# Optimization experiments

Hardware: AMD Instinct MI355X
Metric: run time of the kernel (lower is better)

Reference implementation:

```python
import jax, jax.numpy as jnp
import numpy as np

LEFT = 16  # attention window size (previous `left` symbols incl. current)


def _make_history(symbols, left):
    """contexts[b, t, j] = symbols[b, t - (left-1-j)] for j in [0,left),
    padded with symbols[b, 0] for out-of-range positions (pad = symbols[:, :1])."""
    B, T = symbols.shape
    # (T, left) gather index matrix
    idx = jnp.arange(T)[:, None] - (left - 1 - jnp.arange(left))[None, :]
    valid = idx >= 0
    idx_c = jnp.clip(idx, 0, T - 1)
    ctx = symbols[:, idx_c]                                   # (B, T, left)
    pad = symbols[:, :1][:, :, None]                          # (B, 1, 1)
    return jnp.where(valid[None, :, :], ctx, pad)             # (B, T, left)


def setup_inputs() -> dict:
    key = jax.random.key(0)
    k1, k2, k3, k4 = jax.random.split(key, 4)
    B, T, V, D = 8, 2048, 256, 512
    symbols = jax.random.randint(k1, (B, T), 0, V, dtype=jnp.int32)
    encodings = jax.random.normal(k2, (B, T, D), dtype=jnp.float32)
    # keras 'uniform' initializer: U(-0.05, 0.05)
    M = jax.random.uniform(k3, (V, D), minval=-0.05, maxval=0.05, dtype=jnp.float32)
    C = jax.random.uniform(k4, (V, D), minval=-0.05, maxval=0.05, dtype=jnp.float32)
    return {"symbols": symbols, "encodings": encodings, "M": M, "C": C}


def reference(symbols, encodings, M, C):
    contexts = _make_history(symbols, LEFT)                   # (B, T, L) int
    Mg = M[contexts]                                          # (B, T, L, D)
    Cg = C[contexts]                                          # (B, T, L, D)
    scores = jnp.einsum('btld,btd->btl', Mg, encodings)       # (B, T, L)
    p = jax.nn.softmax(scores, axis=-1)                       # (B, T, L)
    compressed = jnp.einsum('btl,btld->btd', p, Cg)           # (B, T, D)
    output = jnp.concatenate([compressed, encodings], axis=-1)  # (B, T, 2D)
    return output, p
```

## Files before the change

### kernel.cpp

```cpp
#include <hip/hip_runtime.h>
#include <hip/hip_bf16.h>

#define B_ 8
#define T_ 2048
#define V_ 256
#define D_ 512
#define LEFT_ 16

typedef float f32x4 __attribute__((ext_vector_type(4)));
typedef short bf16x8 __attribute__((ext_vector_type(8)));
union FragU { unsigned u[4]; bf16x8 v; };

__device__ __forceinline__ unsigned pack_bf2(float a, float b) {
    __hip_bfloat162 h = __float22bfloat162_rn(make_float2(a, b));
    union { __hip_bfloat162 h; unsigned u; } c; c.h = h; return c.u;
}

__global__ __launch_bounds__(512)
void score_kernel(const int* __restrict__ symbols,
                  const float* __restrict__ encodings,
                  const float* __restrict__ M,
                  float* __restrict__ out,
                  float* __restrict__ p_out) {
    __shared__ __align__(16) float sp[8 * 16 * 36];

    const int tid  = threadIdx.x;
    const int lane = tid & 63;
    const int w    = tid >> 6;
    const int q    = lane >> 4;
    const int t    = lane & 15;

    const int blk = blockIdx.x;
    const int b   = blk >> 7;
    const int t0  = (blk & 127) * 16;
    const int* symrow = symbols + b * T_;
    const size_t rowbase = (size_t)b * T_ + t0;

    int sa[2];
    #pragma unroll
    for (int g = 0; g < 2; ++g) {
        int pos = t0 + t + 16 * g - (LEFT_ - 1);
        pos = max(pos, 0); pos = min(pos, T_ - 1);
        sa[g] = symrow[pos];
    }

    FragU bf[2];
    {
        const float* ebase = encodings + (rowbase + t) * D_;
        float* obase = out + (rowbase + t) * 1024 + D_;
        #pragma unroll
        for (int kc = 0; kc < 2; ++kc) {
            const int d0 = 64 * w + 32 * kc + 4 * q;
            const float4 e0 = *(const float4*)(ebase + d0);
            const float4 e1 = *(const float4*)(ebase + d0 + 16);
            *(float4*)(obase + d0)      = e0;
            *(float4*)(obase + d0 + 16) = e1;
            bf[kc].u[0] = pack_bf2(e0.x, e0.y); bf[kc].u[1] = pack_bf2(e0.z, e0.w);
            bf[kc].u[2] = pack_bf2(e1.x, e1.y); bf[kc].u[3] = pack_bf2(e1.z, e1.w);
        }
    }

    f32x4 acc0 = {0.f, 0.f, 0.f, 0.f}, acc1 = {0.f, 0.f, 0.f, 0.f};
    #pragma unroll
    for (int kc = 0; kc < 2; ++kc) {
        const int k0 = 64 * w + 32 * kc + 4 * q;
        {
            const float* ma = M + (size_t)sa[0] * D_ + k0;
            const float4 x0 = *(const float4*)ma;
            const float4 x1 = *(const float4*)(ma + 16);
            FragU af;
            af.u[0] = pack_bf2(x0.x, x0.y); af.u[1] = pack_bf2(x0.z, x0.w);
            af.u[2] = pack_bf2(x1.x, x1.y); af.u[3] = pack_bf2(x1.z, x1.w);
            acc0 = __builtin_amdgcn_mfma_f32_16x16x32_bf16(af.v, bf[kc].v, acc0, 0, 0, 0);
        }
        {
            const float* ma = M + (size_t)sa[1] * D_ + k0;
            const float4 x0 = *(const float4*)ma;
            const float4 x1 = *(const float4*)(ma + 16);
            FragU af;
            af.u[0] = pack_bf2(x0.x, x0.y); af.u[1] = pack_bf2(x0.z, x0.w);
            af.u[2] = pack_bf2(x1.x, x1.y); af.u[3] = pack_bf2(x1.z, x1.w);
            acc1 = __builtin_amdgcn_mfma_f32_16x16x32_bf16(af.v, bf[kc].v, acc1, 0, 0, 0);
        }
    }
    *(f32x4*)&sp[(w * 16 + t) * 36 + 4 * q]      = acc0;
    *(f32x4*)&sp[(w * 16 + t) * 36 + 16 + 4 * q] = acc1;

    __syncthreads();

    {
        f32x4 s0 = *(const f32x4*)&sp[t * 36 + 4 * q];
        f32x4 s1 = *(const f32x4*)&sp[t * 36 + 16 + 4 * q];
        #pragma unroll
        for (int w2 = 1; w2 < 8; ++w2) {
            s0 += *(const f32x4*)&sp[(w2 * 16 + t) * 36 + 4 * q];
            s1 += *(const f32x4*)&sp[(w2 * 16 + t) * 36 + 16 + 4 * q];
        }
        float mx = -3.0e38f;
        #pragma unroll
        for (int r = 0; r < 4; ++r) {
            if ((unsigned)(4 * q + r - t) < 16u)      mx = fmaxf(mx, s0[r]);
            if ((unsigned)(4 * q + r + 16 - t) < 16u) mx = fmaxf(mx, s1[r]);
        }
        mx = fmaxf(mx, __shfl_xor(mx, 16));
        mx = fmaxf(mx, __shfl_xor(mx, 32));
        float p0[4], p1[4];
        float sum = 0.f;
        #pragma unroll
        for (int r = 0; r < 4; ++r) {
            const bool m0 = (unsigned)(4 * q + r - t) < 16u;
            const bool m1 = (unsigned)(4 * q + r + 16 - t) < 16u;
            p0[r] = m0 ? __expf(s0[r] - mx) : 0.f;
            p1[r] = m1 ? __expf(s1[r] - mx) : 0.f;
            sum += p0[r] + p1[r];
        }
        sum += __shfl_xor(sum, 16);
        sum += __shfl_xor(sum, 32);
        const float inv = 1.f / sum;

        if (w == 0) {
            #pragma unroll
            for (int r = 0; r < 4; ++r) {
                const int j0 = 4 * q + r;
                if ((unsigned)(j0 - t) < 16u)
                    p_out[(rowbase + t) * 16 + (j0 - t)] = p0[r] * inv;
                else
                    p_out[(rowbase + t) * 16 + (j0 + 16 - t)] = p1[r] * inv;
            }
        }
    }
}

__global__ __launch_bounds__(256)
void compress_kernel(const int* __restrict__ symbols,
                     const float* __restrict__ C,
                     const float* __restrict__ p_in,
                     float* __restrict__ out) {
    const int tid  = threadIdx.x;
    const int lane = tid & 63;
    const int w    = tid >> 6;

    const int blk = blockIdx.x;
    const int b   = blk >> 7;
    const int tb  = (blk & 127) * 16 + w * 4;
    const int* symrow = symbols + b * T_;
    const size_t rowbase = (size_t)b * T_ + tb;
    const int dof = lane * 8;

    float pv[4];
    #pragma unroll
    for (int tk = 0; tk < 4; ++tk)
        pv[tk] = p_in[(rowbase + tk) * 16 + (lane & 15)];

    float4 a0[4], a1[4];
    #pragma unroll
    for (int tk = 0; tk < 4; ++tk) {
        a0[tk] = make_float4(0.f, 0.f, 0.f, 0.f);
        a1[tk] = make_float4(0.f, 0.f, 0.f, 0.f);
    }

    #pragma unroll
    for (int i = 0; i < 19; ++i) {
        int pos = tb - (LEFT_ - 1) + i;
        pos = max(pos, 0);
        const int sym = __builtin_amdgcn_readfirstlane(symrow[pos]);
        const float* cr = C + (size_t)sym * D_ + dof;
        const float4 c0 = *(const float4*)cr;
        const float4 c1 = *(const float4*)(cr + 4);
        #pragma unroll
        for (int tk = 0; tk < 4; ++tk) {
            const int sl = i - tk;
            if (sl >= 0 && sl < 16) {
                const float pb = __shfl(pv[tk], sl);
                a0[tk].x += pb * c0.x; a0[tk].y += pb * c0.y;
                a0[tk].z += pb * c0.z; a0[tk].w += pb * c0.w;
                a1[tk].x += pb * c1.x; a1[tk].y += pb * c1.y;
                a1[tk].z += pb * c1.z; a1[tk].w += pb * c1.w;
            }
        }
    }

    #pragma unroll
    for (int tk = 0; tk < 4; ++tk) {
        float* ob = out + (rowbase + tk) * 1024 + dof;
        *(float4*)ob       = a0[tk];
        *(float4*)(ob + 4) = a1[tk];
    }
}

extern "C" void kernel_launch(void* const* d_in, const int* in_sizes, int n_in,
                              void* d_out, int out_size, void* d_ws, size_t ws_size,
                              hipStream_t stream) {
    const int*   symbols   = (const int*)d_in[0];
    const float* encodings = (const float*)d_in[1];
    const float* M         = (const float*)d_in[2];
    const float* C         = (const float*)d_in[3];
    float* out   = (float*)d_out;
    float* p_out = out + (size_t)B_ * T_ * 1024;

    dim3 grid(B_ * (T_ / 16));
    score_kernel<<<grid, 512, 0, stream>>>(symbols, encodings, M, out, p_out);
    compress_kernel<<<grid, 256, 0, stream>>>(symbols, C, p_out, out);
}
```

Baseline: 39.90 us.

## Fuse score/softmax and compress kernels into one per-wave attention kernel

Merges the score and compress kernels into a single launch. Each wave now computes scores for its own 4 timesteps over the full D with 16 MFMA steps, which removes the cross-wave LDS reduction and __syncthreads. The probabilities stay in registers and are broadcast via shuffles into the compress loop, so p no longer round-trips through global memory and one launch is dropped. In exchange, each wave does redundant MFMA work because only 4 of the 16 columns are useful, and it loads more M rows per wave.

```diff
diff --git a/kernel.cpp b/kernel.cpp
--- a/kernel.cpp
+++ b/kernel.cpp
@@ -16,14 +16,13 @@
     union { __hip_bfloat162 h; unsigned u; } c; c.h = h; return c.u;
 }
 
-__global__ __launch_bounds__(512)
-void score_kernel(const int* __restrict__ symbols,
-                  const float* __restrict__ encodings,
-                  const float* __restrict__ M,
-                  float* __restrict__ out,
-                  float* __restrict__ p_out) {
-    __shared__ __align__(16) float sp[8 * 16 * 36];
-
+__global__ __launch_bounds__(256)
+void attn_cell_kernel(const int* __restrict__ symbols,
+                      const float* __restrict__ encodings,
+                      const float* __restrict__ M,
+                      const float* __restrict__ C,
+                      float* __restrict__ out,
+                      float* __restrict__ p_out) {
     const int tid  = threadIdx.x;
     const int lane = tid & 63;
     const int w    = tid >> 6;
@@ -32,125 +31,98 @@
 
     const int blk = blockIdx.x;
     const int b   = blk >> 7;
-    const int t0  = (blk & 127) * 16;
+    const int tb  = (blk & 127) * 16 + w * 4;
     const int* symrow = symbols + b * T_;
-    const size_t rowbase = (size_t)b * T_ + t0;
+    const size_t rowbase = (size_t)b * T_ + tb;
+    const int dof = lane * 8;
 
-    int sa[2];
+    int syms[19];
     #pragma unroll
-    for (int g = 0; g < 2; ++g) {
-        int pos = t0 + t + 16 * g - (LEFT_ - 1);
-        pos = max(pos, 0); pos = min(pos, T_ - 1);
-        sa[g] = symrow[pos];
+    for (int i = 0; i < 19; ++i) {
+        int pos = tb - (LEFT_ - 1) + i;
+        pos = max(pos, 0);
+        syms[i] = __builtin_amdgcn_readfirstlane(symrow[pos]);
     }
 
-    FragU bf[2];
+    #pragma unroll
+    for (int tk = 0; tk < 4; ++tk) {
+        const float* e = encodings + (rowbase + tk) * D_ + dof;
+        const float4 x0 = *(const float4*)e;
+        const float4 x1 = *(const float4*)(e + 4);
+        float* o = out + (rowbase + tk) * 1024 + D_ + dof;
+        *(float4*)o       = x0;
+        *(float4*)(o + 4) = x1;
+    }
+
+    int pos0 = tb - (LEFT_ - 1) + t;  pos0 = max(pos0, 0);
+    int pos1 = tb + 1 + min(t, 2);
+    const int sym0 = symrow[pos0];
+    const int sym1 = symrow[pos1];
+
+    f32x4 acc0 = {0.f, 0.f, 0.f, 0.f}, acc1 = {0.f, 0.f, 0.f, 0.f};
     {
-        const float* ebase = encodings + (rowbase + t) * D_;
-        float* obase = out + (rowbase + t) * 1024 + D_;
+        const float* eb  = encodings + (rowbase + (t & 3)) * D_;
+        const float* ma0 = M + (size_t)sym0 * D_;
+        const float* ma1 = M + (size_t)sym1 * D_;
         #pragma unroll
-        for (int kc = 0; kc < 2; ++kc) {
-            const int d0 = 64 * w + 32 * kc + 4 * q;
-            const float4 e0 = *(const float4*)(ebase + d0);
-            const float4 e1 = *(const float4*)(ebase + d0 + 16);
-            *(float4*)(obase + d0)      = e0;
-            *(float4*)(obase + d0 + 16) = e1;
-            bf[kc].u[0] = pack_bf2(e0.x, e0.y); bf[kc].u[1] = pack_bf2(e0.z, e0.w);
-            bf[kc].u[2] = pack_bf2(e1.x, e1.y); bf[kc].u[3] = pack_bf2(e1.z, e1.w);
+        for (int ks = 0; ks < 16; ++ks) {
+            const int k0 = ks * 32 + 4 * q;
+            const float4 e0 = *(const float4*)(eb + k0);
+            const float4 e1 = *(const float4*)(eb + k0 + 16);
+            FragU bf;
+            bf.u[0] = pack_bf2(e0.x, e0.y); bf.u[1] = pack_bf2(e0.z, e0.w);
+            bf.u[2] = pack_bf2(e1.x, e1.y); bf.u[3] = pack_bf2(e1.z, e1.w);
+            const float4 m00 = *(const float4*)(ma0 + k0);
+            const float4 m01 = *(const float4*)(ma0 + k0 + 16);
+            FragU a0;
+            a0.u[0] = pack_bf2(m00.x, m00.y); a0.u[1] = pack_bf2(m00.z, m00.w);
+            a0.u[2] = pack_bf2(m01.x, m01.y); a0.u[3] = pack_bf2(m01.z, m01.w);
+            const float4 m10 = *(const float4*)(ma1 + k0);
+            const float4 m11 = *(const float4*)(ma1 + k0 + 16);
+            FragU a1;
+            a1.u[0] = pack_bf2(m10.x, m10.y); a1.u[1] = pack_bf2(m10.z, m10.w);
+            a1.u[2] = pack_bf2(m11.x, m11.y); a1.u[3] = pack_bf2(m11.z, m11.w);
+            acc0 = __builtin_amdgcn_mfma_f32_16x16x32_bf16(a0.v, bf.v, acc0, 0, 0, 0);
+            acc1 = __builtin_amdgcn_mfma_f32_16x16x32_bf16(a1.v, bf.v, acc1, 0, 0, 0);
         }
     }
 
-    f32x4 acc0 = {0.f, 0.f, 0.f, 0.f}, acc1 = {0.f, 0.f, 0.f, 0.f};
-    #pragma unroll
-    for (int kc = 0; kc < 2; ++kc) {
-        const int k0 = 64 * w + 32 * kc + 4 * q;
-        {
-            const float* ma = M + (size_t)sa[0] * D_ + k0;
-            const float4 x0 = *(const float4*)ma;
-            const float4 x1 = *(const float4*)(ma + 16);
-            FragU af;
-            af.u[0] = pack_bf2(x0.x, x0.y); af.u[1] = pack_bf2(x0.z, x0.w);
-            af.u[2] = pack_bf2(x1.x, x1.y); af.u[3] = pack_bf2(x1.z, x1.w);
-            acc0 = __builtin_amdgcn_mfma_f32_16x16x32_bf16(af.v, bf[kc].v, acc0, 0, 0, 0);
-        }
-        {
-            const float* ma = M + (size_t)sa[1] * D_ + k0;
-            const float4 x0 = *(const float4*)ma;
-            const float4 x1 = *(const float4*)(ma + 16);
-            FragU af;
-            af.u[0] = pack_bf2(x0.x, x0.y); af.u[1] = pack_bf2(x0.z, x0.w);
-            af.u[2] = pack_bf2(x1.x, x1.y); af.u[3] = pack_bf2(x1.z, x1.w);
-            acc1 = __builtin_amdgcn_mfma_f32_16x16x32_bf16(af.v, bf[kc].v, acc1, 0, 0, 0);
-        }
-    }
-    *(f32x4*)&sp[(w * 16 + t) * 36 + 4 * q]      = acc0;
-    *(f32x4*)&sp[(w * 16 + t) * 36 + 16 + 4 * q] = acc1;
-
-    __syncthreads();
-
+    float p0[4], p1[4];
     {
-        f32x4 s0 = *(const f32x4*)&sp[t * 36 + 4 * q];
-        f32x4 s1 = *(const f32x4*)&sp[t * 36 + 16 + 4 * q];
-        #pragma unroll
-        for (int w2 = 1; w2 < 8; ++w2) {
-            s0 += *(const f32x4*)&sp[(w2 * 16 + t) * 36 + 4 * q];
-            s1 += *(const f32x4*)&sp[(w2 * 16 + t) * 36 + 16 + 4 * q];
-        }
         float mx = -3.0e38f;
         #pragma unroll
         for (int r = 0; r < 4; ++r) {
-            if ((unsigned)(4 * q + r - t) < 16u)      mx = fmaxf(mx, s0[r]);
-            if ((unsigned)(4 * q + r + 16 - t) < 16u) mx = fmaxf(mx, s1[r]);
+            if ((unsigned)(4 * q + r - t) < 16u)      mx = fmaxf(mx, acc0[r]);
+            if ((unsigned)(4 * q + r + 16 - t) < 16u) mx = fmaxf(mx, acc1[r]);
         }
         mx = fmaxf(mx, __shfl_xor(mx, 16));
         mx = fmaxf(mx, __shfl_xor(mx, 32));
-        float p0[4], p1[4];
         float sum = 0.f;
         #pragma unroll
         for (int r = 0; r < 4; ++r) {
             const bool m0 = (unsigned)(4 * q + r - t) < 16u;
             const bool m1 = (unsigned)(4 * q + r + 16 - t) < 16u;
-            p0[r] = m0 ? __expf(s0[r] - mx) : 0.f;
-            p1[r] = m1 ? __expf(s1[r] - mx) : 0.f;
+            p0[r] = m0 ? __expf(acc0[r] - mx) : 0.f;
+            p1[r] = m1 ? __expf(acc1[r] - mx) : 0.f;
             sum += p0[r] + p1[r];
         }
         sum += __shfl_xor(sum, 16);
         sum += __shfl_xor(sum, 32);
         const float inv = 1.f / sum;
+        #pragma unroll
+        for (int r = 0; r < 4; ++r) { p0[r] *= inv; p1[r] *= inv; }
+    }
 
-        if (w == 0) {
-            #pragma unroll
-            for (int r = 0; r < 4; ++r) {
-                const int j0 = 4 * q + r;
-                if ((unsigned)(j0 - t) < 16u)
-                    p_out[(rowbase + t) * 16 + (j0 - t)] = p0[r] * inv;
-                else
-                    p_out[(rowbase + t) * 16 + (j0 + 16 - t)] = p1[r] * inv;
-            }
+    if (t < 4) {
+        #pragma unroll
+        for (int r = 0; r < 4; ++r) {
+            const int j0 = 4 * q + r;
+            if ((unsigned)(j0 - t) < 16u)
+                p_out[(rowbase + t) * 16 + (j0 - t)] = p0[r];
+            else
+                p_out[(rowbase + t) * 16 + (j0 + 16 - t)] = p1[r];
         }
     }
-}
-
-__global__ __launch_bounds__(256)
-void compress_kernel(const int* __restrict__ symbols,
-                     const float* __restrict__ C,
-                     const float* __restrict__ p_in,
-                     float* __restrict__ out) {
-    const int tid  = threadIdx.x;
-    const int lane = tid & 63;
-    const int w    = tid >> 6;
-
-    const int blk = blockIdx.x;
-    const int b   = blk >> 7;
-    const int tb  = (blk & 127) * 16 + w * 4;
-    const int* symrow = symbols + b * T_;
-    const size_t rowbase = (size_t)b * T_ + tb;
-    const int dof = lane * 8;
-
-    float pv[4];
-    #pragma unroll
-    for (int tk = 0; tk < 4; ++tk)
-        pv[tk] = p_in[(rowbase + tk) * 16 + (lane & 15)];
 
     float4 a0[4], a1[4];
     #pragma unroll
@@ -158,20 +130,18 @@
         a0[tk] = make_float4(0.f, 0.f, 0.f, 0.f);
         a1[tk] = make_float4(0.f, 0.f, 0.f, 0.f);
     }
-
     #pragma unroll
     for (int i = 0; i < 19; ++i) {
-        int pos = tb - (LEFT_ - 1) + i;
-        pos = max(pos, 0);
-        const int sym = __builtin_amdgcn_readfirstlane(symrow[pos]);
-        const float* cr = C + (size_t)sym * D_ + dof;
+        const float* cr = C + (size_t)syms[i] * D_ + dof;
         const float4 c0 = *(const float4*)cr;
         const float4 c1 = *(const float4*)(cr + 4);
         #pragma unroll
         for (int tk = 0; tk < 4; ++tk) {
             const int sl = i - tk;
             if (sl >= 0 && sl < 16) {
-                const float pb = __shfl(pv[tk], sl);
+                const int src = ((i & 15) >> 2) * 16 + tk;
+                const float pb = (i >= 16) ? __shfl(p1[i & 3], src)
+                                           : __shfl(p0[i & 3], src);
                 a0[tk].x += pb * c0.x; a0[tk].y += pb * c0.y;
                 a0[tk].z += pb * c0.z; a0[tk].w += pb * c0.w;
                 a1[tk].x += pb * c1.x; a1[tk].y += pb * c1.y;
@@ -199,6 +169,5 @@
     float* p_out = out + (size_t)B_ * T_ * 1024;
 
     dim3 grid(B_ * (T_ / 16));
-    score_kernel<<<grid, 512, 0, stream>>>(symbols, encodings, M, out, p_out);
-    compress_kernel<<<grid, 256, 0, stream>>>(symbols, C, p_out, out);
+    attn_cell_kernel<<<grid, 256, 0, stream>>>(symbols, encodings, M, C, out, p_out);
 }
```

New measurement: 58.18 us. 1.46x slower.
